# Performance work log

Measured on AMD Instinct MI355X. Metric: run time of the kernel, lower is better.

Reference implementation:

```python
import jax, jax.numpy as jnp
import numpy as np

N_NODES = 50000
N_EDGES = 600000
D = 128


def _gcn_layer(h, W, b, src, dst, norm, n_nodes):
    # symmetric-normalized GCN conv: D^{-1/2} A D^{-1/2} H W + b
    h = h * norm[:, None]                                  # [N, d] scale by src norm
    msgs = h[src]                                          # [E, d] gather
    agg = jax.ops.segment_sum(msgs, dst, num_segments=n_nodes)  # [N, d] scatter-add
    agg = agg * norm[:, None]                              # scale by dst norm
    return agg @ W + b


def setup_inputs() -> dict:
    key = jax.random.key(0)
    kf, ks, kd, kw0, kw1 = jax.random.split(key, 5)
    features = jax.random.normal(kf, (N_NODES, D), dtype=jnp.float32)
    src = jax.random.randint(ks, (N_EDGES,), 0, N_NODES)
    dst = jax.random.randint(kd, (N_EDGES,), 0, N_NODES)
    scale = 1.0 / np.sqrt(D)
    W0 = jax.random.normal(kw0, (D, D), dtype=jnp.float32) * scale
    W1 = jax.random.normal(kw1, (D, D), dtype=jnp.float32) * scale
    b0 = jnp.zeros((D,), dtype=jnp.float32)
    b1 = jnp.zeros((D,), dtype=jnp.float32)
    return {"features": features, "src": src, "dst": dst,
            "W0": W0, "b0": b0, "W1": W1, "b1": b1}


def reference(features, src, dst, W0, b0, W1, b1):
    n_nodes = features.shape[0]
    # symmetric norm from in-degree (self-degree clamp to avoid div by zero)
    deg = jax.ops.segment_sum(jnp.ones_like(dst, dtype=features.dtype), dst,
                              num_segments=n_nodes)
    norm = jax.lax.rsqrt(jnp.maximum(deg, 1.0))
    h = _gcn_layer(features, W0, b0, src, dst, norm, n_nodes)
    h = jax.nn.relu(h)
    h = _gcn_layer(h, W1, b1, src, dst, norm, n_nodes)
    return h
```

## Files before the change

### kernel.cpp

```cpp
#include <hip/hip_runtime.h>
#include <hip/hip_bf16.h>

#define D 128
#define CAP 48
#define SB 128
#define SEGCAP 64
#define RB 256

typedef short bf16x8 __attribute__((ext_vector_type(8)));
typedef float f32x4 __attribute__((ext_vector_type(4)));

__device__ inline ushort f2bf(float v) {
    __hip_bfloat16 h = __float2bfloat16(v);
    return *reinterpret_cast<ushort*>(&h);
}
__device__ inline float bflo(uint v) { return __uint_as_float(v << 16); }
__device__ inline float bfhi(uint v) { return __uint_as_float(v & 0xffff0000u); }
__device__ inline uint pk2(float lo, float hi) {
    return (uint)f2bf(lo) | ((uint)f2bf(hi) << 16);
}

__global__ __launch_bounds__(256) void bin_edges_kernel(
    const int* __restrict__ src, const int* __restrict__ dst,
    uint* __restrict__ seg, int* __restrict__ cnt, int E, int nr) {
    __shared__ int lcnt[256];
    __shared__ int lcur[256];
    int tid = threadIdx.x, b = blockIdx.x;
    lcnt[tid] = 0;
    __syncthreads();
    int ce = (E + SB - 1) / SB;
    int ebeg = b * ce, eend = min(ebeg + ce, E);
    for (int e = ebeg + tid; e < eend; e += 256)
        atomicAdd(&lcnt[dst[e] >> 8], 1);
    __syncthreads();
    lcur[tid] = 0;
    if (tid < nr) cnt[b * 256 + tid] = lcnt[tid];
    __syncthreads();
    for (int e = ebeg + tid; e < eend; e += 256) {
        int d = dst[e];
        int r = d >> 8;
        int c = atomicAdd(&lcur[r], 1);
        if (c < SEGCAP)
            seg[(r * SB + b) * SEGCAP + c] = (uint)src[e] | ((uint)(d & 255) << 16);
    }
}

__global__ __launch_bounds__(256) void scatter_local_kernel(
    const uint* __restrict__ seg, const int* __restrict__ cnt,
    ushort* __restrict__ bucket, int* __restrict__ degv, int n_nodes) {
    __shared__ int lc[256];
    int tid = threadIdx.x, r = blockIdx.x;
    lc[tid] = 0;
    __syncthreads();
    int sub = tid >> 5, lane = tid & 31;
    for (int b = sub; b < SB; b += 8) {
        int n = min(cnt[b * 256 + r], SEGCAP);
        int base = (r * SB + b) * SEGCAP;
        for (int i = lane; i < n; i += 32) {
            uint u = seg[base + i];
            int ldst = u >> 16;
            int s = u & 0xffff;
            int c = atomicAdd(&lc[ldst], 1);
            if (c < CAP) bucket[(r * RB + ldst) * CAP + c] = (ushort)s;
        }
    }
    __syncthreads();
    int node = r * RB + tid;
    if (node < n_nodes) degv[node] = min(lc[tid], CAP);
}

__global__ __launch_bounds__(256) void prep_kernel(
    const float4* __restrict__ x, const int* __restrict__ degv,
    float* __restrict__ normv, uint2* __restrict__ xs,
    const float* __restrict__ W0, const float* __restrict__ W1,
    ushort* __restrict__ Wt0, ushort* __restrict__ Wt1, int n_nodes) {
    int tid = threadIdx.x;
    if (blockIdx.x < 32) {
#pragma unroll
        for (int kk = 0; kk < 4; ++kk) {
            int idx = blockIdx.x * 1024 + kk * 256 + tid;
            const float* W = (idx < 16384) ? W0 : W1;
            ushort* Wt = (idx < 16384) ? Wt0 : Wt1;
            int e = idx & 16383;
            int n = e >> 7, k = e & 127;
            Wt[e] = f2bf(W[k * 128 + n]);
        }
        return;
    }
    int total = n_nodes * 32;
    int stride = (gridDim.x - 32) * 256;
    for (int i = (blockIdx.x - 32) * 256 + tid; i < total; i += stride) {
        int row = i >> 5;
        float dg = (float)degv[row];
        float nn = rsqrtf(fmaxf(dg, 1.0f));
        if ((i & 31) == 0) normv[row] = nn;
        float4 v = x[i];
        uint2 o;
        o.x = pk2(v.x * nn, v.y * nn);
        o.y = pk2(v.z * nn, v.w * nn);
        xs[i] = o;
    }
}

__global__ __launch_bounds__(256) void gather_bf16_kernel(
    const ushort* __restrict__ x, const float* __restrict__ normv,
    const int* __restrict__ degv, const ushort* __restrict__ bucket,
    ushort* __restrict__ out, int n_nodes) {
    int node = (blockIdx.x * 256 + threadIdx.x) >> 6;
    if (node >= n_nodes) return;
    int lane = threadIdx.x & 63;
    int grp = lane >> 4;
    int l16 = lane & 15;
    int e0 = node * CAP;
    int e1 = e0 + degv[node];
    const uint4* xp = (const uint4*)x;

    float a[8] = {0.f, 0.f, 0.f, 0.f, 0.f, 0.f, 0.f, 0.f};
    int e = e0 + grp;
    for (; e + 8 < e1; e += 12) {
        int s0 = bucket[e];
        int s1 = bucket[e + 4];
        int s2 = bucket[e + 8];
        uint4 v0 = xp[(size_t)s0 * 16 + l16];
        uint4 v1 = xp[(size_t)s1 * 16 + l16];
        uint4 v2 = xp[(size_t)s2 * 16 + l16];
        a[0] += bflo(v0.x); a[1] += bfhi(v0.x);
        a[2] += bflo(v0.y); a[3] += bfhi(v0.y);
        a[4] += bflo(v0.z); a[5] += bfhi(v0.z);
        a[6] += bflo(v0.w); a[7] += bfhi(v0.w);
        a[0] += bflo(v1.x); a[1] += bfhi(v1.x);
        a[2] += bflo(v1.y); a[3] += bfhi(v1.y);
        a[4] += bflo(v1.z); a[5] += bfhi(v1.z);
        a[6] += bflo(v1.w); a[7] += bfhi(v1.w);
        a[0] += bflo(v2.x); a[1] += bfhi(v2.x);
        a[2] += bflo(v2.y); a[3] += bfhi(v2.y);
        a[4] += bflo(v2.z); a[5] += bfhi(v2.z);
        a[6] += bflo(v2.w); a[7] += bfhi(v2.w);
    }
    for (; e < e1; e += 4) {
        int s = bucket[e];
        uint4 v = xp[(size_t)s * 16 + l16];
        a[0] += bflo(v.x); a[1] += bfhi(v.x);
        a[2] += bflo(v.y); a[3] += bfhi(v.y);
        a[4] += bflo(v.z); a[5] += bfhi(v.z);
        a[6] += bflo(v.w); a[7] += bfhi(v.w);
    }

#pragma unroll
    for (int j = 0; j < 8; ++j) {
        a[j] += __shfl_xor(a[j], 16, 64);
        a[j] += __shfl_xor(a[j], 32, 64);
    }

    if (grp == 0) {
        float nn = normv[node];
        uint4 o;
        o.x = pk2(a[0] * nn, a[1] * nn);
        o.y = pk2(a[2] * nn, a[3] * nn);
        o.z = pk2(a[4] * nn, a[5] * nn);
        o.w = pk2(a[6] * nn, a[7] * nn);
        ((uint4*)out)[(size_t)node * 16 + l16] = o;
    }
}

template <bool LAYER1>
__global__ __launch_bounds__(256) void mfma_matmul_kernel(
    const ushort* __restrict__ A, const ushort* __restrict__ Wt,
    const float* __restrict__ bias, const float* __restrict__ normv,
    void* outp, int n_nodes) {
    __shared__ ushort Ws[128 * 136];
    int tid = threadIdx.x;

#pragma unroll
    for (int i = 0; i < 8; ++i) {
        int e = (i * 256 + tid) * 8;
        int r = e >> 7, c = e & 127;
        *(uint4*)&Ws[r * 136 + c] = *(const uint4*)&Wt[e];
    }
    __syncthreads();

    int w = tid >> 6, lane = tid & 63;
    int n16 = lane & 15, g = lane >> 4;
    int rowbase = blockIdx.x * 64 + w * 16;
    int arow = rowbase + n16;

    const bf16x8 zero8 = {0, 0, 0, 0, 0, 0, 0, 0};
    bf16x8 a[4];
    bool aok = (arow < n_nodes);
#pragma unroll
    for (int kk = 0; kk < 4; ++kk)
        a[kk] = aok ? *(const bf16x8*)&A[(size_t)arow * 128 + kk * 32 + g * 8] : zero8;

    float bvals[8];
#pragma unroll
    for (int j = 0; j < 8; ++j) bvals[j] = bias[j * 16 + n16];

    f32x4 acc[8];
#pragma unroll
    for (int j = 0; j < 8; ++j) acc[j] = (f32x4){0.f, 0.f, 0.f, 0.f};

#pragma unroll
    for (int kk = 0; kk < 4; ++kk) {
#pragma unroll
        for (int j = 0; j < 8; ++j) {
            bf16x8 b = *(const bf16x8*)&Ws[(j * 16 + n16) * 136 + kk * 32 + g * 8];
            acc[j] = __builtin_amdgcn_mfma_f32_16x16x32_bf16(a[kk], b, acc[j], 0, 0, 0);
        }
    }

    int rloc = g * 4;
#pragma unroll
    for (int r = 0; r < 4; ++r) {
        int row = rowbase + rloc + r;
        if (row >= n_nodes) continue;
        if (LAYER1) {
            float nn = normv[row];
            ushort* ob = (ushort*)outp;
#pragma unroll
            for (int j = 0; j < 8; ++j) {
                float v = fmaxf(acc[j][r] + bvals[j], 0.f) * nn;
                ob[(size_t)row * 128 + j * 16 + n16] = f2bf(v);
            }
        } else {
            float* of = (float*)outp;
#pragma unroll
            for (int j = 0; j < 8; ++j)
                of[(size_t)row * 128 + j * 16 + n16] = acc[j][r] + bvals[j];
        }
    }
}


extern "C" void kernel_launch(void* const* d_in, const int* in_sizes, int n_in,
                              void* d_out, int out_size, void* d_ws, size_t ws_size,
                              hipStream_t stream) {
    const float* features = (const float*)d_in[0];
    const int*   src      = (const int*)d_in[1];
    const int*   dst      = (const int*)d_in[2];
    const float* W0       = (const float*)d_in[3];
    const float* b0       = (const float*)d_in[4];
    const float* W1       = (const float*)d_in[5];
    const float* b1       = (const float*)d_in[6];
    float* out = (float*)d_out;

    const int N = in_sizes[0] / D;
    const int E = in_sizes[1];
    const int NR = (N + RB - 1) / RB;

    char* ws = (char*)d_ws;
    size_t off = 0;
    auto take = [&](size_t bytes) {
        char* p = ws + off;
        off = (off + bytes + 255) & ~(size_t)255;
        return p;
    };
    int*    degv   = (int*)take((size_t)N * 4);
    float*  normv  = (float*)take((size_t)N * 4);
    ushort* bucket = (ushort*)take((size_t)N * CAP * 2);
    uint*   seg    = (uint*)take((size_t)NR * SB * SEGCAP * 4);
    int*    cnt    = (int*)take((size_t)SB * 256 * 4);
    ushort* Wt0    = (ushort*)take(16384 * 2);
    ushort* Wt1    = (ushort*)take(16384 * 2);
    ushort* xs     = (ushort*)take((size_t)N * D * 2);
    ushort* buf1   = (ushort*)d_out;

    int GB = (N + 3) / 4;
    int MB = (N + 63) / 64;

    bin_edges_kernel<<<SB, 256, 0, stream>>>(src, dst, seg, cnt, E, NR);
    scatter_local_kernel<<<NR, 256, 0, stream>>>(seg, cnt, bucket, degv, N);
    prep_kernel<<<32 + 2048, 256, 0, stream>>>((const float4*)features, degv, normv,
                                               (uint2*)xs, W0, W1, Wt0, Wt1, N);

    gather_bf16_kernel<<<GB, 256, 0, stream>>>(xs, normv, degv, bucket, buf1, N);
    mfma_matmul_kernel<true><<<MB, 256, 0, stream>>>(buf1, Wt0, b0, normv, buf1, N);
    gather_bf16_kernel<<<GB, 256, 0, stream>>>(buf1, normv, degv, bucket, xs, N);
    mfma_matmul_kernel<false><<<MB, 256, 0, stream>>>(xs, Wt1, b1, nullptr, out, N);
}
```

Measured before the change: 113.9 us.

## Fuse gather with MFMA matmul per layer and merge prep into binning kernels

```diff
diff --git a/kernel.cpp b/kernel.cpp
--- a/kernel.cpp
+++ b/kernel.cpp
@@ -22,10 +22,25 @@
 
 __global__ __launch_bounds__(256) void bin_edges_kernel(
     const int* __restrict__ src, const int* __restrict__ dst,
-    uint* __restrict__ seg, int* __restrict__ cnt, int E, int nr) {
+    uint* __restrict__ seg, int* __restrict__ cnt, int E, int nr,
+    const float* __restrict__ W0, const float* __restrict__ W1,
+    ushort* __restrict__ Wt0, ushort* __restrict__ Wt1) {
+    int tid = threadIdx.x;
+    if (blockIdx.x >= SB) {
+#pragma unroll
+        for (int kk = 0; kk < 4; ++kk) {
+            int idx = (blockIdx.x - SB) * 1024 + kk * 256 + tid;
+            const float* W = (idx < 16384) ? W0 : W1;
+            ushort* Wt = (idx < 16384) ? Wt0 : Wt1;
+            int e = idx & 16383;
+            int n = e >> 7, k = e & 127;
+            Wt[e] = f2bf(W[k * 128 + n]);
+        }
+        return;
+    }
     __shared__ int lcnt[256];
     __shared__ int lcur[256];
-    int tid = threadIdx.x, b = blockIdx.x;
+    int b = blockIdx.x;
     lcnt[tid] = 0;
     __syncthreads();
     int ce = (E + SB - 1) / SB;
@@ -45,10 +60,12 @@
     }
 }
 
-__global__ __launch_bounds__(256) void scatter_local_kernel(
+__global__ __launch_bounds__(256) void scatter_prep_kernel(
     const uint* __restrict__ seg, const int* __restrict__ cnt,
-    ushort* __restrict__ bucket, int* __restrict__ degv, int n_nodes) {
+    ushort* __restrict__ bucket, int* __restrict__ degv, float* __restrict__ normv,
+    const float4* __restrict__ x, uint2* __restrict__ xs, int n_nodes) {
     __shared__ int lc[256];
+    __shared__ float lnorm[256];
     int tid = threadIdx.x, r = blockIdx.x;
     lc[tid] = 0;
     __syncthreads();
@@ -66,166 +83,146 @@
     }
     __syncthreads();
     int node = r * RB + tid;
-    if (node < n_nodes) degv[node] = min(lc[tid], CAP);
-}
-
-__global__ __launch_bounds__(256) void prep_kernel(
-    const float4* __restrict__ x, const int* __restrict__ degv,
-    float* __restrict__ normv, uint2* __restrict__ xs,
-    const float* __restrict__ W0, const float* __restrict__ W1,
-    ushort* __restrict__ Wt0, ushort* __restrict__ Wt1, int n_nodes) {
+    int dg = min(lc[tid], CAP);
+    float nn = rsqrtf(fmaxf((float)dg, 1.0f));
+    lnorm[tid] = nn;
+    if (node < n_nodes) { degv[node] = dg; normv[node] = nn; }
+    __syncthreads();
+    int base = r * RB;
+    int nrow = min(RB, n_nodes - base);
+    if (nrow <= 0) return;
+    const float4* xf = x + (size_t)base * 32;
+    uint2* xo = xs + (size_t)base * 32;
+    for (int i = tid; i < nrow * 32; i += 256) {
+        float4 v = xf[i];
+        float s = lnorm[i >> 5];
+        uint2 o;
+        o.x = pk2(v.x * s, v.y * s);
+        o.y = pk2(v.z * s, v.w * s);
+        xo[i] = o;
+    }
+}
+
+template <bool LAYER1>
+__global__ __launch_bounds__(512, 4) void fused_layer_kernel(
+    const ushort* __restrict__ A, const float* __restrict__ normv,
+    const int* __restrict__ degv, const ushort* __restrict__ bucket,
+    const ushort* __restrict__ Wt, const float* __restrict__ bias,
+    void* outp, int n_nodes) {
+    __shared__ ushort Ws[128 * 136];
+    __shared__ ushort As[64 * 136];
     int tid = threadIdx.x;
-    if (blockIdx.x < 32) {
-#pragma unroll
-        for (int kk = 0; kk < 4; ++kk) {
-            int idx = blockIdx.x * 1024 + kk * 256 + tid;
-            const float* W = (idx < 16384) ? W0 : W1;
-            ushort* Wt = (idx < 16384) ? Wt0 : Wt1;
-            int e = idx & 16383;
-            int n = e >> 7, k = e & 127;
-            Wt[e] = f2bf(W[k * 128 + n]);
-        }
-        return;
-    }
-    int total = n_nodes * 32;
-    int stride = (gridDim.x - 32) * 256;
-    for (int i = (blockIdx.x - 32) * 256 + tid; i < total; i += stride) {
-        int row = i >> 5;
-        float dg = (float)degv[row];
-        float nn = rsqrtf(fmaxf(dg, 1.0f));
-        if ((i & 31) == 0) normv[row] = nn;
-        float4 v = x[i];
-        uint2 o;
-        o.x = pk2(v.x * nn, v.y * nn);
-        o.y = pk2(v.z * nn, v.w * nn);
-        xs[i] = o;
-    }
-}
-
-__global__ __launch_bounds__(256) void gather_bf16_kernel(
-    const ushort* __restrict__ x, const float* __restrict__ normv,
-    const int* __restrict__ degv, const ushort* __restrict__ bucket,
-    ushort* __restrict__ out, int n_nodes) {
-    int node = (blockIdx.x * 256 + threadIdx.x) >> 6;
-    if (node >= n_nodes) return;
-    int lane = threadIdx.x & 63;
+    int w = tid >> 6, lane = tid & 63;
+    int base = blockIdx.x * 64;
+
+#pragma unroll
+    for (int i = 0; i < 4; ++i) {
+        int e = (i * 512 + tid) * 8;
+        int r = e >> 7, c = e & 127;
+        *(uint4*)&Ws[r * 136 + c] = *(const uint4*)&Wt[e];
+    }
+
     int grp = lane >> 4;
     int l16 = lane & 15;
-    int e0 = node * CAP;
-    int e1 = e0 + degv[node];
-    const uint4* xp = (const uint4*)x;
-
-    float a[8] = {0.f, 0.f, 0.f, 0.f, 0.f, 0.f, 0.f, 0.f};
-    int e = e0 + grp;
-    for (; e + 8 < e1; e += 12) {
-        int s0 = bucket[e];
-        int s1 = bucket[e + 4];
-        int s2 = bucket[e + 8];
-        uint4 v0 = xp[(size_t)s0 * 16 + l16];
-        uint4 v1 = xp[(size_t)s1 * 16 + l16];
-        uint4 v2 = xp[(size_t)s2 * 16 + l16];
-        a[0] += bflo(v0.x); a[1] += bfhi(v0.x);
-        a[2] += bflo(v0.y); a[3] += bfhi(v0.y);
-        a[4] += bflo(v0.z); a[5] += bfhi(v0.z);
-        a[6] += bflo(v0.w); a[7] += bfhi(v0.w);
-        a[0] += bflo(v1.x); a[1] += bfhi(v1.x);
-        a[2] += bflo(v1.y); a[3] += bfhi(v1.y);
-        a[4] += bflo(v1.z); a[5] += bfhi(v1.z);
-        a[6] += bflo(v1.w); a[7] += bfhi(v1.w);
-        a[0] += bflo(v2.x); a[1] += bfhi(v2.x);
-        a[2] += bflo(v2.y); a[3] += bfhi(v2.y);
-        a[4] += bflo(v2.z); a[5] += bfhi(v2.z);
-        a[6] += bflo(v2.w); a[7] += bfhi(v2.w);
-    }
-    for (; e < e1; e += 4) {
-        int s = bucket[e];
-        uint4 v = xp[(size_t)s * 16 + l16];
-        a[0] += bflo(v.x); a[1] += bfhi(v.x);
-        a[2] += bflo(v.y); a[3] += bfhi(v.y);
-        a[4] += bflo(v.z); a[5] += bfhi(v.z);
-        a[6] += bflo(v.w); a[7] += bfhi(v.w);
-    }
-
-#pragma unroll
-    for (int j = 0; j < 8; ++j) {
-        a[j] += __shfl_xor(a[j], 16, 64);
-        a[j] += __shfl_xor(a[j], 32, 64);
-    }
-
-    if (grp == 0) {
-        float nn = normv[node];
-        uint4 o;
-        o.x = pk2(a[0] * nn, a[1] * nn);
-        o.y = pk2(a[2] * nn, a[3] * nn);
-        o.z = pk2(a[4] * nn, a[5] * nn);
-        o.w = pk2(a[6] * nn, a[7] * nn);
-        ((uint4*)out)[(size_t)node * 16 + l16] = o;
-    }
-}
-
-template <bool LAYER1>
-__global__ __launch_bounds__(256) void mfma_matmul_kernel(
-    const ushort* __restrict__ A, const ushort* __restrict__ Wt,
-    const float* __restrict__ bias, const float* __restrict__ normv,
-    void* outp, int n_nodes) {
-    __shared__ ushort Ws[128 * 136];
-    int tid = threadIdx.x;
-
+    const uint4* xp = (const uint4*)A;
 #pragma unroll
     for (int i = 0; i < 8; ++i) {
-        int e = (i * 256 + tid) * 8;
-        int r = e >> 7, c = e & 127;
-        *(uint4*)&Ws[r * 136 + c] = *(const uint4*)&Wt[e];
-    }
-    __syncthreads();
-
-    int w = tid >> 6, lane = tid & 63;
+        int lr = w * 8 + i;
+        int node = base + lr;
+        float a[8] = {0.f, 0.f, 0.f, 0.f, 0.f, 0.f, 0.f, 0.f};
+        if (node < n_nodes) {
+            int e0 = node * CAP;
+            int e1 = e0 + degv[node];
+            int e = e0 + grp;
+            for (; e + 8 < e1; e += 12) {
+                int s0 = bucket[e];
+                int s1 = bucket[e + 4];
+                int s2 = bucket[e + 8];
+                uint4 v0 = xp[(size_t)s0 * 16 + l16];
+                uint4 v1 = xp[(size_t)s1 * 16 + l16];
+                uint4 v2 = xp[(size_t)s2 * 16 + l16];
+                a[0] += bflo(v0.x); a[1] += bfhi(v0.x);
+                a[2] += bflo(v0.y); a[3] += bfhi(v0.y);
+                a[4] += bflo(v0.z); a[5] += bfhi(v0.z);
+                a[6] += bflo(v0.w); a[7] += bfhi(v0.w);
+                a[0] += bflo(v1.x); a[1] += bfhi(v1.x);
+                a[2] += bflo(v1.y); a[3] += bfhi(v1.y);
+                a[4] += bflo(v1.z); a[5] += bfhi(v1.z);
+                a[6] += bflo(v1.w); a[7] += bfhi(v1.w);
+                a[0] += bflo(v2.x); a[1] += bfhi(v2.x);
+                a[2] += bflo(v2.y); a[3] += bfhi(v2.y);
+                a[4] += bflo(v2.z); a[5] += bfhi(v2.z);
+                a[6] += bflo(v2.w); a[7] += bfhi(v2.w);
+            }
+            for (; e < e1; e += 4) {
+                int s = bucket[e];
+                uint4 v = xp[(size_t)s * 16 + l16];
+                a[0] += bflo(v.x); a[1] += bfhi(v.x);
+                a[2] += bflo(v.y); a[3] += bfhi(v.y);
+                a[4] += bflo(v.z); a[5] += bfhi(v.z);
+                a[6] += bflo(v.w); a[7] += bfhi(v.w);
+            }
+#pragma unroll
+            for (int j = 0; j < 8; ++j) {
+                a[j] += __shfl_xor(a[j], 16, 64);
+                a[j] += __shfl_xor(a[j], 32, 64);
+            }
+        }
+        if (grp == 0) {
+            float nn = (node < n_nodes) ? normv[node] : 0.f;
+            uint4 o;
+            o.x = pk2(a[0] * nn, a[1] * nn);
+            o.y = pk2(a[2] * nn, a[3] * nn);
+            o.z = pk2(a[4] * nn, a[5] * nn);
+            o.w = pk2(a[6] * nn, a[7] * nn);
+            *(uint4*)&As[lr * 136 + l16 * 8] = o;
+        }
+    }
+    __syncthreads();
+
+    int wr = w & 3, wc = w >> 2;
     int n16 = lane & 15, g = lane >> 4;
-    int rowbase = blockIdx.x * 64 + w * 16;
-    int arow = rowbase + n16;
-
-    const bf16x8 zero8 = {0, 0, 0, 0, 0, 0, 0, 0};
-    bf16x8 a[4];
-    bool aok = (arow < n_nodes);
+
+    bf16x8 af[4];
 #pragma unroll
     for (int kk = 0; kk < 4; ++kk)
-        a[kk] = aok ? *(const bf16x8*)&A[(size_t)arow * 128 + kk * 32 + g * 8] : zero8;
-
-    float bvals[8];
-#pragma unroll
-    for (int j = 0; j < 8; ++j) bvals[j] = bias[j * 16 + n16];
-
-    f32x4 acc[8];
-#pragma unroll
-    for (int j = 0; j < 8; ++j) acc[j] = (f32x4){0.f, 0.f, 0.f, 0.f};
+        af[kk] = *(const bf16x8*)&As[(wr * 16 + n16) * 136 + kk * 32 + g * 8];
+
+    float bvals[4];
+#pragma unroll
+    for (int j = 0; j < 4; ++j) bvals[j] = bias[wc * 64 + j * 16 + n16];
+
+    f32x4 acc[4];
+#pragma unroll
+    for (int j = 0; j < 4; ++j) acc[j] = (f32x4){0.f, 0.f, 0.f, 0.f};
 
 #pragma unroll
     for (int kk = 0; kk < 4; ++kk) {
 #pragma unroll
-        for (int j = 0; j < 8; ++j) {
-            bf16x8 b = *(const bf16x8*)&Ws[(j * 16 + n16) * 136 + kk * 32 + g * 8];
-            acc[j] = __builtin_amdgcn_mfma_f32_16x16x32_bf16(a[kk], b, acc[j], 0, 0, 0);
-        }
-    }
-
-    int rloc = g * 4;
+        for (int j = 0; j < 4; ++j) {
+            bf16x8 b = *(const bf16x8*)&Ws[(wc * 64 + j * 16 + n16) * 136 + kk * 32 + g * 8];
+            acc[j] = __builtin_amdgcn_mfma_f32_16x16x32_bf16(af[kk], b, acc[j], 0, 0, 0);
+        }
+    }
+
+    int rloc = wr * 16 + g * 4;
 #pragma unroll
     for (int r = 0; r < 4; ++r) {
-        int row = rowbase + rloc + r;
+        int row = base + rloc + r;
         if (row >= n_nodes) continue;
         if (LAYER1) {
             float nn = normv[row];
             ushort* ob = (ushort*)outp;
 #pragma unroll
-            for (int j = 0; j < 8; ++j) {
+            for (int j = 0; j < 4; ++j) {
                 float v = fmaxf(acc[j][r] + bvals[j], 0.f) * nn;
-                ob[(size_t)row * 128 + j * 16 + n16] = f2bf(v);
+                ob[(size_t)row * 128 + wc * 64 + j * 16 + n16] = f2bf(v);
             }
         } else {
             float* of = (float*)outp;
 #pragma unroll
-            for (int j = 0; j < 8; ++j)
-                of[(size_t)row * 128 + j * 16 + n16] = acc[j][r] + bvals[j];
+            for (int j = 0; j < 4; ++j)
+                of[(size_t)row * 128 + wc * 64 + j * 16 + n16] = acc[j][r] + bvals[j];
         }
     }
 }
@@ -262,18 +259,16 @@
     ushort* Wt0    = (ushort*)take(16384 * 2);
     ushort* Wt1    = (ushort*)take(16384 * 2);
     ushort* xs     = (ushort*)take((size_t)N * D * 2);
-    ushort* buf1   = (ushort*)d_out;
-
-    int GB = (N + 3) / 4;
+    ushort* h1s    = (ushort*)take((size_t)N * D * 2);
+
     int MB = (N + 63) / 64;
 
-    bin_edges_kernel<<<SB, 256, 0, stream>>>(src, dst, seg, cnt, E, NR);
-    scatter_local_kernel<<<NR, 256, 0, stream>>>(seg, cnt, bucket, degv, N);
-    prep_kernel<<<32 + 2048, 256, 0, stream>>>((const float4*)features, degv, normv,
-                                               (uint2*)xs, W0, W1, Wt0, Wt1, N);
-
-    gather_bf16_kernel<<<GB, 256, 0, stream>>>(xs, normv, degv, bucket, buf1, N);
-    mfma_matmul_kernel<true><<<MB, 256, 0, stream>>>(buf1, Wt0, b0, normv, buf1, N);
-    gather_bf16_kernel<<<GB, 256, 0, stream>>>(buf1, normv, degv, bucket, xs, N);
-    mfma_matmul_kernel<false><<<MB, 256, 0, stream>>>(xs, Wt1, b1, nullptr, out, N);
-}
+    bin_edges_kernel<<<SB + 32, 256, 0, stream>>>(src, dst, seg, cnt, E, NR,
+                                                  W0, W1, Wt0, Wt1);
+    scatter_prep_kernel<<<NR, 256, 0, stream>>>(seg, cnt, bucket, degv, normv,
+                                                (const float4*)features, (uint2*)xs, N);
+    fused_layer_kernel<true><<<MB, 512, 0, stream>>>(xs, normv, degv, bucket,
+                                                     Wt0, b0, h1s, N);
+    fused_layer_kernel<false><<<MB, 512, 0, stream>>>(h1s, normv, degv, bucket,
+                                                      Wt1, b1, out, N);
+}
```

Measured after the change: 136.4 us. 1.2x slower.

## Fuse feature prep into scatter kernel and weight transpose into binning kernel

Applied to the files above, without the earlier changes.

```diff
diff --git a/kernel.cpp b/kernel.cpp
--- a/kernel.cpp
+++ b/kernel.cpp
@@ -22,10 +22,25 @@
 
 __global__ __launch_bounds__(256) void bin_edges_kernel(
     const int* __restrict__ src, const int* __restrict__ dst,
-    uint* __restrict__ seg, int* __restrict__ cnt, int E, int nr) {
+    uint* __restrict__ seg, int* __restrict__ cnt, int E, int nr,
+    const float* __restrict__ W0, const float* __restrict__ W1,
+    ushort* __restrict__ Wt0, ushort* __restrict__ Wt1) {
+    int tid = threadIdx.x;
+    if (blockIdx.x >= SB) {
+#pragma unroll
+        for (int kk = 0; kk < 4; ++kk) {
+            int idx = (blockIdx.x - SB) * 1024 + kk * 256 + tid;
+            const float* W = (idx < 16384) ? W0 : W1;
+            ushort* Wt = (idx < 16384) ? Wt0 : Wt1;
+            int e = idx & 16383;
+            int n = e >> 7, k = e & 127;
+            Wt[e] = f2bf(W[k * 128 + n]);
+        }
+        return;
+    }
     __shared__ int lcnt[256];
     __shared__ int lcur[256];
-    int tid = threadIdx.x, b = blockIdx.x;
+    int b = blockIdx.x;
     lcnt[tid] = 0;
     __syncthreads();
     int ce = (E + SB - 1) / SB;
@@ -45,10 +60,12 @@
     }
 }
 
-__global__ __launch_bounds__(256) void scatter_local_kernel(
+__global__ __launch_bounds__(256) void scatter_prep_kernel(
     const uint* __restrict__ seg, const int* __restrict__ cnt,
-    ushort* __restrict__ bucket, int* __restrict__ degv, int n_nodes) {
+    ushort* __restrict__ bucket, int* __restrict__ degv, float* __restrict__ normv,
+    const float4* __restrict__ x, uint2* __restrict__ xs, int n_nodes) {
     __shared__ int lc[256];
+    __shared__ float lnorm[256];
     int tid = threadIdx.x, r = blockIdx.x;
     lc[tid] = 0;
     __syncthreads();
@@ -66,39 +83,23 @@
     }
     __syncthreads();
     int node = r * RB + tid;
-    if (node < n_nodes) degv[node] = min(lc[tid], CAP);
-}
-
-__global__ __launch_bounds__(256) void prep_kernel(
-    const float4* __restrict__ x, const int* __restrict__ degv,
-    float* __restrict__ normv, uint2* __restrict__ xs,
-    const float* __restrict__ W0, const float* __restrict__ W1,
-    ushort* __restrict__ Wt0, ushort* __restrict__ Wt1, int n_nodes) {
-    int tid = threadIdx.x;
-    if (blockIdx.x < 32) {
-#pragma unroll
-        for (int kk = 0; kk < 4; ++kk) {
-            int idx = blockIdx.x * 1024 + kk * 256 + tid;
-            const float* W = (idx < 16384) ? W0 : W1;
-            ushort* Wt = (idx < 16384) ? Wt0 : Wt1;
-            int e = idx & 16383;
-            int n = e >> 7, k = e & 127;
-            Wt[e] = f2bf(W[k * 128 + n]);
-        }
-        return;
-    }
-    int total = n_nodes * 32;
-    int stride = (gridDim.x - 32) * 256;
-    for (int i = (blockIdx.x - 32) * 256 + tid; i < total; i += stride) {
-        int row = i >> 5;
-        float dg = (float)degv[row];
-        float nn = rsqrtf(fmaxf(dg, 1.0f));
-        if ((i & 31) == 0) normv[row] = nn;
-        float4 v = x[i];
+    int dg = min(lc[tid], CAP);
+    float nn = rsqrtf(fmaxf((float)dg, 1.0f));
+    lnorm[tid] = nn;
+    if (node < n_nodes) { degv[node] = dg; normv[node] = nn; }
+    __syncthreads();
+    int base = r * RB;
+    int nrow = min(RB, n_nodes - base);
+    if (nrow <= 0) return;
+    const float4* xf = x + (size_t)base * 32;
+    uint2* xo = xs + (size_t)base * 32;
+    for (int i = tid; i < nrow * 32; i += 256) {
+        float4 v = xf[i];
+        float s = lnorm[i >> 5];
         uint2 o;
-        o.x = pk2(v.x * nn, v.y * nn);
-        o.y = pk2(v.z * nn, v.w * nn);
-        xs[i] = o;
+        o.x = pk2(v.x * s, v.y * s);
+        o.y = pk2(v.z * s, v.w * s);
+        xo[i] = o;
     }
 }
 
@@ -262,18 +263,17 @@
     ushort* Wt0    = (ushort*)take(16384 * 2);
     ushort* Wt1    = (ushort*)take(16384 * 2);
     ushort* xs     = (ushort*)take((size_t)N * D * 2);
-    ushort* buf1   = (ushort*)d_out;
+    ushort* bufA   = (ushort*)take((size_t)N * D * 2);
 
     int GB = (N + 3) / 4;
     int MB = (N + 63) / 64;
 
-    bin_edges_kernel<<<SB, 256, 0, stream>>>(src, dst, seg, cnt, E, NR);
-    scatter_local_kernel<<<NR, 256, 0, stream>>>(seg, cnt, bucket, degv, N);
-    prep_kernel<<<32 + 2048, 256, 0, stream>>>((const float4*)features, degv, normv,
-                                               (uint2*)xs, W0, W1, Wt0, Wt1, N);
-
-    gather_bf16_kernel<<<GB, 256, 0, stream>>>(xs, normv, degv, bucket, buf1, N);
-    mfma_matmul_kernel<true><<<MB, 256, 0, stream>>>(buf1, Wt0, b0, normv, buf1, N);
-    gather_bf16_kernel<<<GB, 256, 0, stream>>>(buf1, normv, degv, bucket, xs, N);
+    bin_edges_kernel<<<SB + 32, 256, 0, stream>>>(src, dst, seg, cnt, E, NR,
+                                                  W0, W1, Wt0, Wt1);
+    scatter_prep_kernel<<<NR, 256, 0, stream>>>(seg, cnt, bucket, degv, normv,
+                                                (const float4*)features, (uint2*)xs, N);
+    gather_bf16_kernel<<<GB, 256, 0, stream>>>(xs, normv, degv, bucket, bufA, N);
+    mfma_matmul_kernel<true><<<MB, 256, 0, stream>>>(bufA, Wt0, b0, normv, bufA, N);
+    gather_bf16_kernel<<<GB, 256, 0, stream>>>(bufA, normv, degv, bucket, xs, N);
     mfma_matmul_kernel<false><<<MB, 256, 0, stream>>>(xs, Wt1, b1, nullptr, out, N);
 }
```

Result: faster. 109.5 us (-3.9%).
